# Performance work log

Measured on AMD Instinct MI355X. Metric: run time of the kernel, lower is better.

Reference implementation:

```python
import jax, jax.numpy as jnp
import numpy as np

B, L, D, KD, H = 4, 2048, 512, 64, 8


def _dequant(w_int, scale, zp):
    # per-tensor asymmetric dequantization: (q - zero_point) * scale
    return (w_int.astype(jnp.float32) - zp) * scale


def setup_inputs() -> dict:
    key = jax.random.key(0)
    ks = jax.random.split(key, 20)
    inp = {
        'query': jax.random.normal(ks[0], (B, L, D), jnp.float32),
        'key':   jax.random.normal(ks[1], (B, L, D), jnp.float32),
        'value': jax.random.normal(ks[2], (B, L, D), jnp.float32),
        'wq_q': jax.random.randint(ks[3], (D, KD, H), 0, 127, jnp.int32),
        'wk_q': jax.random.randint(ks[4], (D, KD, H), 0, 127, jnp.int32),
        'wv_q': jax.random.randint(ks[5], (D, KD, H), 0, 127, jnp.int32),
        'wo_q': jax.random.randint(ks[6], (KD * H, D), 0, 127, jnp.int32),
        'bq': jax.random.normal(ks[7], (KD, H), jnp.float32) * 0.02,
        'bk': jax.random.normal(ks[8], (KD, H), jnp.float32) * 0.02,
        'bv': jax.random.normal(ks[9], (KD, H), jnp.float32) * 0.02,
        'bo': jax.random.normal(ks[10], (D,), jnp.float32) * 0.02,
        'scale_q': jax.random.uniform(ks[11], (), jnp.float32, 0.001, 0.01),
        'scale_k': jax.random.uniform(ks[12], (), jnp.float32, 0.001, 0.01),
        'scale_v': jax.random.uniform(ks[13], (), jnp.float32, 0.001, 0.01),
        'scale_o': jax.random.uniform(ks[14], (), jnp.float32, 0.001, 0.01),
        'zp_q': jax.random.uniform(ks[15], (), jnp.float32, 50.0, 70.0),
        'zp_k': jax.random.uniform(ks[16], (), jnp.float32, 50.0, 70.0),
        'zp_v': jax.random.uniform(ks[17], (), jnp.float32, 50.0, 70.0),
        'zp_o': jax.random.uniform(ks[18], (), jnp.float32, 50.0, 70.0),
    }
    return inp


def reference(query, key, value, wq_q, wk_q, wv_q, wo_q, bq, bk, bv, bo,
              scale_q, scale_k, scale_v, scale_o, zp_q, zp_k, zp_v, zp_o):
    # Dequantize int8 weights (quantized-inference path of the layer)
    wq = _dequant(wq_q, scale_q, zp_q)  # (D, KD, H)
    wk = _dequant(wk_q, scale_k, zp_k)
    wv = _dequant(wv_q, scale_v, zp_v)
    wo = _dequant(wo_q, scale_o, zp_o)  # (KD*H, D)

    q = jnp.einsum('bij,jkh->bikh', query, wq) + bq  # (B, L, KD, H)
    k = jnp.einsum('bij,jkh->bikh', key,   wk) + bk
    v = jnp.einsum('bij,jkh->bikh', value, wv) + bv

    # scores: contract over key_dim -> (B, Lq, Lk, H)
    scores = jnp.einsum('bidh,bjdh->bijh', q, k) / jnp.sqrt(jnp.float32(KD))
    # tf softmax over axis=-2 of bikh == key axis (axis 2 here)
    attn = jax.nn.softmax(scores, axis=2)
    out = jnp.einsum('bijh,bjdh->bidh', attn, v)  # (B, L, KD, H)
    out = out.reshape(out.shape[0], out.shape[1], KD * H)  # flatten (d,h) row-major, same as tf.reshape
    return jnp.matmul(out, wo) + bo
```

## Files before the change

kernel.cpp:

```cpp
#include <hip/hip_runtime.h>
#include <math.h>
#include <stdint.h>

#define BB 4
#define LL 2048
#define DD 512
#define KDIM 64
#define HH 8

typedef _Float16 f16;
typedef f16 f16x8 __attribute__((ext_vector_type(8)));
typedef f16 f16x4v __attribute__((ext_vector_type(4)));
typedef float f32x4 __attribute__((ext_vector_type(4)));

__device__ __forceinline__ int swz7(int x) { return x ^ (((x >> 7) & 7) << 4); }
__device__ __forceinline__ int swz8(int x) { return x ^ (((x >> 8) & 7) << 4); }

__device__ __forceinline__ void gload16(const void* g, void* l) {
    __builtin_amdgcn_global_load_lds(
        (const __attribute__((address_space(1))) void*)g,
        (__attribute__((address_space(3))) void*)l, 16, 0, 0);
}

__device__ __forceinline__ void wait_barrier() {
    asm volatile("s_waitcnt vmcnt(0)" ::: "memory");
    __builtin_amdgcn_s_barrier();
}

__global__ __launch_bounds__(256)
void prologue(const int* __restrict__ w0, const int* __restrict__ w1,
              const int* __restrict__ w2, const int* __restrict__ w3,
              const float* s0, const float* s1, const float* s2, const float* s3,
              const float* z0, const float* z1, const float* z2, const float* z3,
              f16* o0, f16* o1, f16* o2, f16* o3,
              const float* __restrict__ xq, const float* __restrict__ xk,
              const float* __restrict__ xv, f16* cq, f16* ck, f16* cv)
{
    __shared__ float t[32][33];
    const int bid = blockIdx.x;
    if (bid < 1024) {
        const int zi = bid >> 8, rem = bid & 255;
        const int* W = zi == 0 ? w0 : zi == 1 ? w1 : zi == 2 ? w2 : w3;
        const float sc = *(zi == 0 ? s0 : zi == 1 ? s1 : zi == 2 ? s2 : s3);
        const float zp = *(zi == 0 ? z0 : zi == 1 ? z1 : zi == 2 ? z2 : z3);
        f16* WT = zi == 0 ? o0 : zi == 1 ? o1 : zi == 2 ? o2 : o3;
        const int n0 = (rem & 15) * 32, k0 = (rem >> 4) * 32;
        const int x = threadIdx.x & 31, y = threadIdx.x >> 5;
        #pragma unroll
        for (int i = 0; i < 32; i += 8)
            t[y + i][x] = ((float)W[(size_t)(k0 + y + i) * DD + n0 + x] - zp) * sc;
        __syncthreads();
        if (zi == 3) {
            const int k = k0 + x;
            const int kp = (k & 7) * 64 + (k >> 3);
            #pragma unroll
            for (int i = 0; i < 32; i += 8)
                WT[(size_t)(n0 + y + i) * DD + kp] = (f16)t[x][y + i];
        } else {
            #pragma unroll
            for (int i = 0; i < 32; i += 8)
                WT[(size_t)(n0 + y + i) * DD + k0 + x] = (f16)t[x][y + i];
        }
    } else {
        const int c = bid - 1024;
        const int yi = c >> 12, xb = c & 4095;
        const float* in = yi == 0 ? xq : yi == 1 ? xk : xv;
        f16* out = yi == 0 ? cq : yi == 1 ? ck : cv;
        const int i = (xb * 256 + threadIdx.x) * 4;
        float4 v = *(const float4*)(in + i);
        f16x4v o = {(f16)v.x, (f16)v.y, (f16)v.z, (f16)v.w};
        *(f16x4v*)(out + i) = o;
    }
}

template<int EPI>
__device__ __forceinline__
void gemm_body(char* As, char* Bs, const f16* __restrict__ A,
               const f16* __restrict__ BT, const float* __restrict__ bias,
               void* __restrict__ OutP)
{
    const int tid = threadIdx.x, lane = tid & 63, wid = tid >> 6;
    const int g = lane >> 4, ql = lane & 15;
    const int wm = wid >> 1, wn = wid & 1;
    const int bid = blockIdx.x;
    const int sb = (bid & 7) * 32 + (bid >> 3);
    const int rowBase = (sb >> 2) * 128, colBase = (sb & 3) * 128;

    auto stage = [&](int p, int buf) {
        const int kt = p * 32;
        #pragma unroll
        for (int i = 0; i < 2; ++i) {
            const int xl = i * 4096 + wid * 1024 + lane * 16;
            const int xs = swz7(xl);
            const int r = xs >> 6, cb = xs & 63;
            const char* asrc;
            if (EPI == 1) {
                const int m = rowBase + r, b = m >> 11, qq = m & 2047;
                const int kp = kt * 2 + cb;
                asrc = (const char*)A +
                       (((size_t)((b * 8 + (kp >> 7)) * 2048 + qq)) << 7) + (kp & 127);
            } else {
                asrc = (const char*)(A + (size_t)(rowBase + r) * DD + kt) + cb;
            }
            gload16(asrc, As + buf * 8192 + xl);
            gload16((const char*)(BT + (size_t)(colBase + r) * DD + kt) + cb,
                    Bs + buf * 8192 + xl);
        }
    };

    const f32x4 zero = {0.f, 0.f, 0.f, 0.f};
    f32x4 acc[4][4];
    #pragma unroll
    for (int i = 0; i < 4; ++i)
        #pragma unroll
        for (int j = 0; j < 4; ++j) acc[i][j] = zero;

    stage(0, 0);

    for (int p = 0; p < 16; ++p) {
        const int buf = p & 1;
        wait_barrier();
        if (p < 15) stage(p + 1, buf ^ 1);
        const char* as = As + buf * 8192;
        const char* bs = Bs + buf * 8192;
        f16x8 af[4], bf[4];
        #pragma unroll
        for (int mf = 0; mf < 4; ++mf)
            af[mf] = *(const f16x8*)(as + swz7((wm * 64 + mf * 16 + ql) * 64 + g * 16));
        #pragma unroll
        for (int nf = 0; nf < 4; ++nf)
            bf[nf] = *(const f16x8*)(bs + swz7((wn * 64 + nf * 16 + ql) * 64 + g * 16));
        __builtin_amdgcn_s_setprio(1);
        #pragma unroll
        for (int mf = 0; mf < 4; ++mf)
            #pragma unroll
            for (int nf = 0; nf < 4; ++nf)
                acc[mf][nf] = __builtin_amdgcn_mfma_f32_16x16x32_f16(af[mf], bf[nf], acc[mf][nf], 0, 0, 0);
        __builtin_amdgcn_s_setprio(0);
    }

    #pragma unroll
    for (int nf = 0; nf < 4; ++nf) {
        const int n = colBase + wn * 64 + nf * 16 + ql;
        const float bn = bias[n];
        #pragma unroll
        for (int mf = 0; mf < 4; ++mf) {
            const int m0 = rowBase + wm * 64 + mf * 16 + g * 4;
            if (EPI == 2) {
                const int b = m0 >> 11, l0 = m0 & 2047;
                const int kd = n >> 3, hh = n & 7;
                f16x4v o = {(f16)(acc[mf][nf][0] + bn), (f16)(acc[mf][nf][1] + bn),
                            (f16)(acc[mf][nf][2] + bn), (f16)(acc[mf][nf][3] + bn)};
                *(f16x4v*)((f16*)OutP + ((size_t)(b * HH + hh) * KDIM + kd) * LL + l0) = o;
            } else {
                #pragma unroll
                for (int r = 0; r < 4; ++r) {
                    const int m = m0 + r;
                    const float v = acc[mf][nf][r] + bn;
                    if (EPI == 0) {
                        const int b = m >> 11, lr = m & 2047;
                        const int kd = n >> 3, hh = n & 7;
                        ((f16*)OutP)[((size_t)(b * HH + hh) * LL + lr) * KDIM + kd] = (f16)v;
                    } else {
                        ((float*)OutP)[(size_t)m * DD + n] = v;
                    }
                }
            }
        }
    }
}

__global__ __launch_bounds__(256)
void gemm_qkv(const f16* Xq, const f16* Xk, const f16* Xv,
              const f16* WTq, const f16* WTk, const f16* WTv,
              const float* bq, const float* bk, const float* bv,
              f16* Qh, f16* Kh, f16* VhT)
{
    __shared__ __align__(16) char As[2 * 128 * 32 * 2];
    __shared__ __align__(16) char Bs[2 * 128 * 32 * 2];
    const int z = blockIdx.z;
    if (z == 0)      gemm_body<0>(As, Bs, Xq, WTq, bq, Qh);
    else if (z == 1) gemm_body<0>(As, Bs, Xk, WTk, bk, Kh);
    else             gemm_body<2>(As, Bs, Xv, WTv, bv, VhT);
}

__global__ __launch_bounds__(256)
void gemm_out(const f16* A, const f16* BT, const float* bias, float* Out)
{
    __shared__ __align__(16) char As[2 * 128 * 32 * 2];
    __shared__ __align__(16) char Bs[2 * 128 * 32 * 2];
    gemm_body<1>(As, Bs, A, BT, bias, Out);
}

__global__ __launch_bounds__(512, 4)
void attn_f16(const f16* __restrict__ Qh, const f16* __restrict__ Kh,
              const f16* __restrict__ VhT, f16* __restrict__ Ob)
{
    __shared__ __align__(16) char k_s[128 * 128];
    __shared__ __align__(16) char v_s[64 * 256];
    __shared__ __align__(16) char p_s[8 * 4096];

    const int tid = threadIdx.x, lane = tid & 63, wid = tid >> 6;
    const int g = lane >> 4, ql = lane & 15;
    char* pw = p_s + wid * 4096;

    const int bid = blockIdx.x;
    const int sb = (bid & 7) * 64 + (bid >> 3);
    const int qt = sb & 15, bh = sb >> 4;

    const f16*  Qb = Qh + (size_t)bh * LL * KDIM;
    const char* Kb = (const char*)(Kh + (size_t)bh * LL * KDIM);
    const char* Vb = (const char*)(VhT + (size_t)bh * KDIM * LL);
    const int q0 = qt * 128 + wid * 16;

    auto stage = [&](int t) {
        #pragma unroll
        for (int i = 0; i < 2; ++i) {
            const int xl = i * 8192 + wid * 1024 + lane * 16;
            gload16(Kb + (size_t)t * 16384 + swz7(xl), k_s + xl);
            const int xv = swz8(xl);
            gload16(Vb + (size_t)(xl >> 8) * (LL * 2) + t * 256 + (xv & 255),
                    v_s + xl);
        }
    };

    const f16 qscale = (f16)(0.125f * 1.44269504089f);
    f16x8 qfr[2];
    #pragma unroll
    for (int kb = 0; kb < 2; ++kb) {
        qfr[kb] = *(const f16x8*)(Qb + (size_t)(q0 + ql) * KDIM + kb * 32 + g * 8);
        qfr[kb] *= qscale;
    }

    const f32x4 zero = {0.f, 0.f, 0.f, 0.f};
    f32x4 acc[4];
    #pragma unroll
    for (int n = 0; n < 4; ++n) acc[n] = zero;
    float m_r = -1e30f, l_r = 0.f;

    for (int t = 0; t < 16; ++t) {
        stage(t);
        __syncthreads();

        f32x4 s[8];
        __builtin_amdgcn_s_setprio(1);
        #pragma unroll
        for (int kf = 0; kf < 8; ++kf) {
            f16x8 kfr0 = *(const f16x8*)(k_s + swz7((kf * 16 + ql) * 128 + g * 16));
            f16x8 kfr1 = *(const f16x8*)(k_s + swz7((kf * 16 + ql) * 128 + 64 + g * 16));
            f32x4 z = zero;
            z = __builtin_amdgcn_mfma_f32_16x16x32_f16(kfr0, qfr[0], z, 0, 0, 0);
            z = __builtin_amdgcn_mfma_f32_16x16x32_f16(kfr1, qfr[1], z, 0, 0, 0);
            s[kf] = z;
        }
        __builtin_amdgcn_s_setprio(0);

        float t8[8];
        #pragma unroll
        for (int kf = 0; kf < 8; ++kf)
            t8[kf] = fmaxf(fmaxf(s[kf][0], s[kf][1]), fmaxf(s[kf][2], s[kf][3]));
        float mx = fmaxf(fmaxf(fmaxf(t8[0], t8[1]), fmaxf(t8[2], t8[3])),
                         fmaxf(fmaxf(t8[4], t8[5]), fmaxf(t8[6], t8[7])));
        mx = fmaxf(mx, __shfl_xor(mx, 16));
        mx = fmaxf(mx, __shfl_xor(mx, 32));
        if (__any(mx > m_r + 8.f)) {
            const float mnew = fmaxf(m_r, mx);
            const float fsc = exp2f(m_r - mnew);
            m_r = mnew;
            l_r *= fsc;
            #pragma unroll
            for (int n = 0; n < 4; ++n) acc[n] *= fsc;
        }
        float ps = 0.f;
        #pragma unroll
        for (int kf = 0; kf < 8; ++kf) {
            const float p0 = exp2f(s[kf][0] - m_r);
            const float p1 = exp2f(s[kf][1] - m_r);
            const float p2 = exp2f(s[kf][2] - m_r);
            const float p3 = exp2f(s[kf][3] - m_r);
            ps += (p0 + p1) + (p2 + p3);
            f16x4v pk = {(f16)p0, (f16)p1, (f16)p2, (f16)p3};
            *(f16x4v*)(pw + swz8(ql * 256 + kf * 32 + g * 8)) = pk;
        }
        l_r += ps;

        __builtin_amdgcn_s_setprio(1);
        #pragma unroll
        for (int kb = 0; kb < 4; ++kb) {
            f16x8 pf = *(const f16x8*)(pw + swz8(ql * 256 + kb * 64 + g * 16));
            #pragma unroll
            for (int n = 0; n < 4; ++n) {
                f16x8 vf = *(const f16x8*)(v_s + swz8((n * 16 + ql) * 256
                                                      + kb * 64 + g * 16));
                acc[n] = __builtin_amdgcn_mfma_f32_16x16x32_f16(vf, pf, acc[n], 0, 0, 0);
            }
        }
        __builtin_amdgcn_s_setprio(0);
        __syncthreads();
    }

    l_r += __shfl_xor(l_r, 16);
    l_r += __shfl_xor(l_r, 32);
    const float inv = 1.f / l_r;
    const int q = q0 + ql;
    f16* orow = Ob + ((size_t)bh * LL + q) * KDIM;
    #pragma unroll
    for (int n = 0; n < 4; ++n) {
        f16x4v o = {(f16)(acc[n][0] * inv), (f16)(acc[n][1] * inv),
                    (f16)(acc[n][2] * inv), (f16)(acc[n][3] * inv)};
        *(f16x4v*)(orow + n * 16 + g * 4) = o;
    }
}

extern "C" void kernel_launch(void* const* d_in, const int* in_sizes, int n_in,
                              void* d_out, int out_size, void* d_ws, size_t ws_size,
                              hipStream_t stream)
{
    const float* query = (const float*)d_in[0];
    const float* key   = (const float*)d_in[1];
    const float* value = (const float*)d_in[2];
    const int* wq = (const int*)d_in[3];
    const int* wk = (const int*)d_in[4];
    const int* wv = (const int*)d_in[5];
    const int* wo = (const int*)d_in[6];
    const float* bq = (const float*)d_in[7];
    const float* bk = (const float*)d_in[8];
    const float* bv = (const float*)d_in[9];
    const float* bo = (const float*)d_in[10];
    const float* scale_q = (const float*)d_in[11];
    const float* scale_k = (const float*)d_in[12];
    const float* scale_v = (const float*)d_in[13];
    const float* scale_o = (const float*)d_in[14];
    const float* zp_q = (const float*)d_in[15];
    const float* zp_k = (const float*)d_in[16];
    const float* zp_v = (const float*)d_in[17];
    const float* zp_o = (const float*)d_in[18];

    const size_t MD = (size_t)BB * LL * DD;
    const size_t WT_SZ = (size_t)DD * DD;

    f16* Xq  = (f16*)d_ws;
    f16* Xk  = Xq + MD;
    f16* Xv  = Xk + MD;
    f16* WTq = Xv + MD;
    f16* WTk = WTq + WT_SZ;
    f16* WTv = WTk + WT_SZ;
    f16* WTo = WTv + WT_SZ;
    f16* Qh  = WTo + WT_SZ;
    f16* Kh  = Qh + MD;
    f16* VhT = Kh + MD;
    f16* Ob  = VhT + MD;

    prologue<<<1024 + 3 * 4096, 256, 0, stream>>>(
        wq, wk, wv, wo, scale_q, scale_k, scale_v, scale_o,
        zp_q, zp_k, zp_v, zp_o, WTq, WTk, WTv, WTo,
        query, key, value, Xq, Xk, Xv);

    dim3 gg(256, 1, 3);
    gemm_qkv<<<gg, 256, 0, stream>>>(Xq, Xk, Xv, WTq, WTk, WTv,
                                     bq, bk, bv, Qh, Kh, VhT);

    attn_f16<<<512, 512, 0, stream>>>(Qh, Kh, VhT, Ob);

    gemm_out<<<256, 256, 0, stream>>>(Ob, WTo, bo, (float*)d_out);
}
```

Measured before the change: 141.3 us.

## Prefetch next K tile into registers and split V load barrier in attention

```diff
diff --git a/kernel.cpp b/kernel.cpp
--- a/kernel.cpp
+++ b/kernel.cpp
@@ -202,7 +202,6 @@
 
     const int tid = threadIdx.x, lane = tid & 63, wid = tid >> 6;
     const int g = lane >> 4, ql = lane & 15;
-    char* pw = p_s + wid * 4096;
 
     const int bid = blockIdx.x;
     const int sb = (bid & 7) * 64 + (bid >> 3);
@@ -213,16 +212,27 @@
     const char* Vb = (const char*)(VhT + (size_t)bh * KDIM * LL);
     const int q0 = qt * 128 + wid * 16;
 
-    auto stage = [&](int t) {
-        #pragma unroll
-        for (int i = 0; i < 2; ++i) {
-            const int xl = i * 8192 + wid * 1024 + lane * 16;
-            gload16(Kb + (size_t)t * 16384 + swz7(xl), k_s + xl);
-            const int xv = swz8(xl);
-            gload16(Vb + (size_t)(xl >> 8) * (LL * 2) + t * 256 + (xv & 255),
-                    v_s + xl);
-        }
-    };
+    const int xl0 = wid * 1024 + lane * 16;
+    const int xl1 = 8192 + wid * 1024 + lane * 16;
+    const char* ks0 = Kb + swz7(xl0);
+    const char* ks1 = Kb + swz7(xl1);
+    const char* vs0 = Vb + (xl0 >> 8) * (LL * 2) + (swz8(xl0) & 255);
+    const char* vs1 = Vb + (xl1 >> 8) * (LL * 2) + (swz8(xl1) & 255);
+    char* kd0 = k_s + xl0;  char* kd1 = k_s + xl1;
+    char* vd0 = v_s + xl0;  char* vd1 = v_s + xl1;
+
+    const char* kb0 = k_s + swz7(ql * 128 + g * 16);
+    const char* kb1 = k_s + swz7(ql * 128 + 64 + g * 16);
+    char* pw = p_s + wid * 4096;
+    const char* vbs[4]; const char* prs[4]; char* pwa[8];
+    #pragma unroll
+    for (int kb = 0; kb < 4; ++kb) {
+        vbs[kb] = v_s + swz8(ql * 256 + kb * 64 + g * 16);
+        prs[kb] = pw  + swz8(ql * 256 + kb * 64 + g * 16);
+    }
+    #pragma unroll
+    for (int kf = 0; kf < 8; ++kf)
+        pwa[kf] = pw + swz8(ql * 256 + kf * 32 + g * 8);
 
     const f16 qscale = (f16)(0.125f * 1.44269504089f);
     f16x8 qfr[2];
@@ -238,16 +248,27 @@
     for (int n = 0; n < 4; ++n) acc[n] = zero;
     float m_r = -1e30f, l_r = 0.f;
 
+    f16x8 kreg0 = *(const f16x8*)ks0;
+    f16x8 kreg1 = *(const f16x8*)ks1;
+
     for (int t = 0; t < 16; ++t) {
-        stage(t);
-        __syncthreads();
+        *(f16x8*)kd0 = kreg0;
+        *(f16x8*)kd1 = kreg1;
+        asm volatile("s_waitcnt lgkmcnt(0)" ::: "memory");
+        __builtin_amdgcn_s_barrier();
+
+        gload16(vs0 + t * 256, vd0);
+        gload16(vs1 + t * 256, vd1);
+        const int tn = (t + 1) & 15;
+        kreg0 = *(const f16x8*)(ks0 + tn * 16384);
+        kreg1 = *(const f16x8*)(ks1 + tn * 16384);
 
         f32x4 s[8];
         __builtin_amdgcn_s_setprio(1);
         #pragma unroll
         for (int kf = 0; kf < 8; ++kf) {
-            f16x8 kfr0 = *(const f16x8*)(k_s + swz7((kf * 16 + ql) * 128 + g * 16));
-            f16x8 kfr1 = *(const f16x8*)(k_s + swz7((kf * 16 + ql) * 128 + 64 + g * 16));
+            f16x8 kfr0 = *(const f16x8*)(kb0 + kf * 2048);
+            f16x8 kfr1 = *(const f16x8*)(kb1 + kf * 2048);
             f32x4 z = zero;
             z = __builtin_amdgcn_mfma_f32_16x16x32_f16(kfr0, qfr[0], z, 0, 0, 0);
             z = __builtin_amdgcn_mfma_f32_16x16x32_f16(kfr1, qfr[1], z, 0, 0, 0);
@@ -280,23 +301,24 @@
             const float p3 = exp2f(s[kf][3] - m_r);
             ps += (p0 + p1) + (p2 + p3);
             f16x4v pk = {(f16)p0, (f16)p1, (f16)p2, (f16)p3};
-            *(f16x4v*)(pw + swz8(ql * 256 + kf * 32 + g * 8)) = pk;
+            *(f16x4v*)pwa[kf] = pk;
         }
         l_r += ps;
 
+        asm volatile("s_waitcnt vmcnt(0)" ::: "memory");
+        __builtin_amdgcn_s_barrier();
+
         __builtin_amdgcn_s_setprio(1);
         #pragma unroll
         for (int kb = 0; kb < 4; ++kb) {
-            f16x8 pf = *(const f16x8*)(pw + swz8(ql * 256 + kb * 64 + g * 16));
+            f16x8 pf = *(const f16x8*)prs[kb];
             #pragma unroll
             for (int n = 0; n < 4; ++n) {
-                f16x8 vf = *(const f16x8*)(v_s + swz8((n * 16 + ql) * 256
-                                                      + kb * 64 + g * 16));
+                f16x8 vf = *(const f16x8*)(vbs[kb] + n * 4096);
                 acc[n] = __builtin_amdgcn_mfma_f32_16x16x32_f16(vf, pf, acc[n], 0, 0, 0);
             }
         }
         __builtin_amdgcn_s_setprio(0);
-        __syncthreads();
     }
 
     l_r += __shfl_xor(l_r, 16);
```

Measured after the change: 140.6 us. Within noise of the previous version (-0.5%).
